# Kernel tuning notes

Hardware: AMD Instinct MI355X
Metric: run time of the kernel (lower is better)

Reference implementation:

```python
import jax, jax.numpy as jnp
import numpy as np

U = 356  # LSTM units

def _lstm(x, W, Wr, b, h0, c0):
    """Keras-style LSTM. x: [B,T,F]. Returns (hs [B,T,U], h [B,U], c [B,U])."""
    def step(carry, xt):
        h, c = carry
        z = xt @ W + h @ Wr + b            # [B, 4U], gate order i,f,g,o
        i, f, g, o = jnp.split(z, 4, axis=-1)
        c = jax.nn.sigmoid(f) * c + jax.nn.sigmoid(i) * jnp.tanh(g)
        h = jax.nn.sigmoid(o) * jnp.tanh(c)
        return (h, c), h
    (h, c), hs = jax.lax.scan(step, (h0, c0), jnp.swapaxes(x, 0, 1))
    return jnp.swapaxes(hs, 0, 1), h, c


def setup_inputs() -> dict:
    key = jax.random.key(0)
    ks = jax.random.split(key, 12)
    s = 0.05
    return {
        "x": jax.random.normal(ks[0], (8192, 7, 69), jnp.float32),
        "m": jax.random.normal(ks[1], (8192, 7, 45), jnp.float32),
        "enc_W": jax.random.normal(ks[2], (69, 4 * U), jnp.float32) * s,
        "enc_U": jax.random.normal(ks[3], (U, 4 * U), jnp.float32) * s,
        "enc_b": jnp.zeros((4 * U,), jnp.float32),
        "dec_W": jax.random.normal(ks[4], (45, 4 * U), jnp.float32) * s,
        "dec_U": jax.random.normal(ks[5], (U, 4 * U), jnp.float32) * s,
        "dec_b": jnp.zeros((4 * U,), jnp.float32),
        "W_map": jax.random.normal(ks[6], (7 * U, 1024), jnp.float32) * s,
        "b_map": jnp.zeros((1024,), jnp.float32),
        "W1": jax.random.normal(ks[7], (1024, 1024), jnp.float32) * s,
        "b1": jnp.zeros((1024,), jnp.float32),
        "W2": jax.random.normal(ks[8], (1024, 1024), jnp.float32) * s,
        "b2": jnp.zeros((1024,), jnp.float32),
        "W3": jax.random.normal(ks[9], (1024, 1024), jnp.float32) * s,
        "b3": jnp.zeros((1024,), jnp.float32),
        "W_out": jax.random.normal(ks[10], (1024, 168), jnp.float32) * s,
        "b_out": jnp.zeros((168,), jnp.float32),
    }


def reference(x, m, enc_W, enc_U, enc_b, dec_W, dec_U, dec_b,
              W_map, b_map, W1, b1, W2, b2, W3, b3, W_out, b_out):
    B = x.shape[0]
    h0 = jnp.zeros((B, U), x.dtype)
    c0 = jnp.zeros((B, U), x.dtype)
    # Encoder: only final states are used (dropout layers are identity at inference).
    _, s_h, s_c = _lstm(x, enc_W, enc_U, enc_b, h0, c0)
    # Decoder seeded with encoder states, returns full sequence [B,7,U].
    decoded, _, _ = _lstm(m, dec_W, dec_U, dec_b, s_h, s_c)
    f = decoded.reshape(B, -1)                     # [B, 7*356]
    h = jax.nn.relu(f @ W_map + b_map)
    h = jnp.tanh(h @ W1 + b1)
    h = jnp.tanh(h @ W2 + b2)
    h = jnp.tanh(h @ W3 + b3)
    return h @ W_out + b_out                        # [B, 168]
```

## Files before the change

### kernel.cpp

```cpp
#include <hip/hip_runtime.h>
#include <math.h>


using bf16x8 = __attribute__((ext_vector_type(8))) short;
using f32x4  = __attribute__((ext_vector_type(4))) float;

enum { EPI_NONE = 0, EPI_RELU = 1, EPI_TANH = 2 };

__device__ inline unsigned short f2bf(float f) {
    union { float f; unsigned u; } v; v.f = f;
    unsigned r = v.u + 0x7FFFu + ((v.u >> 16) & 1u);
    return (unsigned short)(r >> 16);
}
__device__ inline float sigf(float x) {
    return __fdividef(1.f, 1.f + __expf(-x));
}
__device__ inline float tanhfast(float x) {
    return 1.f - __fdividef(2.f, 1.f + __expf(2.f * x));
}

__device__ inline void gll16(const void* g, void* l) {
    __builtin_amdgcn_global_load_lds(
        (const __attribute__((address_space(1))) unsigned int*)(uintptr_t)g,
        (__attribute__((address_space(3))) unsigned int*)(unsigned int)(uintptr_t)l,
        16, 0, 0);
}

#define PROWS 32
#define PLDA  456

#define STAGEW(kkv)                                                            \
    _Pragma("unroll")                                                          \
    for (int r = 0; r < 12; ++r)                                               \
        gll16(Wt + (size_t)(kkv) * 49152 + (tid + r * 512) * 8,                \
              (void*)&Bs[(tid + r * 512) * 8]);

#define LOADB_LDS(dst)                                                         \
    _Pragma("unroll")                                                          \
    for (int ni = 0; ni < 12; ++ni)                                            \
        dst[ni] = *(const bf16x8*)&Bs[(w * 12 + ni) * 512 + lane * 8];

#define LOADA(dst, kkv)                                                        \
    _Pragma("unroll")                                                          \
    for (int mi = 0; mi < 2; ++mi)                                             \
        dst[mi] = *(const bf16x8*)&Ab[(mi * 16 + lm) * PLDA + (kkv) * 32       \
                                      + quad * 8];

#define MFMA12(aF, bW)                                                         \
    _Pragma("unroll")                                                          \
    for (int ni = 0; ni < 12; ++ni) {                                          \
        acc[0][ni] = __builtin_amdgcn_mfma_f32_16x16x32_bf16(                  \
            aF[0], bW[ni], acc[0][ni], 0, 0, 0);                               \
        acc[1][ni] = __builtin_amdgcn_mfma_f32_16x16x32_bf16(                  \
            aF[1], bW[ni], acc[1][ni], 0, 0, 0);                               \
    }

__global__ __attribute__((amdgpu_flat_work_group_size(512, 512),
                          amdgpu_waves_per_eu(2, 2)))
void lstm_persist(const float* __restrict__ x,
                  const float* __restrict__ m,
                  const unsigned short* __restrict__ WtE,
                  const unsigned short* __restrict__ WtD,
                  const float* __restrict__ bIE,
                  const float* __restrict__ bID,
                  unsigned short* __restrict__ dcd)
{
    __shared__ __attribute__((aligned(16))) unsigned short Ab[PROWS * PLDA];
    __shared__ __attribute__((aligned(16))) unsigned short Bs[49152];
    const int tid  = threadIdx.x;
    const int lane = tid & 63;
    const int w    = tid >> 6;
    const int lm   = lane & 15, quad = lane >> 4;
    const int brow = blockIdx.x * PROWS;
    const int kk0  = blockIdx.x % 14;

    for (int i = tid; i < PROWS * PLDA; i += 512) Ab[i] = 0;
    __syncthreads();
    for (int i = tid; i < PROWS * 69; i += 512) {
        const int r = i / 69, f = i - r * 69;
        Ab[r * PLDA + f] = f2bf(x[((size_t)(brow + r) * 7 + 0) * 69 + f]);
    }

    float creg[2][3][4] = {};
    float bI[3][4];

    for (int s = 0; s < 14; ++s) {
        const bool enc = (s < 7);
        const int t = enc ? s : s - 7;
        const unsigned short* Wt = enc ? WtE : WtD;

        if (s == 0 || s == 7) {
            const float* bsrc = enc ? bIE : bID;
            #pragma unroll
            for (int a = 0; a < 3; ++a)
                #pragma unroll
                for (int g = 0; g < 4; ++g)
                    bI[a][g] = bsrc[(3 * w + a) * 64 + g * 16 + lm];
        }

        STAGEW(kk0)
        __syncthreads();

        f32x4 acc[2][12] = {};
        #pragma unroll 1
        for (int kk = 0; kk < 14; ++kk) {
            const int kks = kk + kk0 - ((kk + kk0 >= 14) ? 14 : 0);
            bf16x8 bR[12], aF[2];
            LOADB_LDS(bR)
            LOADA(aF, kks)
            __syncthreads();
            if (kk < 13) {
                const int kkn = (kks == 13) ? 0 : kks + 1;
                STAGEW(kkn)
            }
            MFMA12(aF, bR)
            if (kk < 13) __syncthreads();
        }

        const int hoff = (s < 6) ? 69 : 45;
        #pragma unroll
        for (int mi = 0; mi < 2; ++mi)
            #pragma unroll
            for (int a = 0; a < 3; ++a) {
                const int u = (3 * w + a) * 16 + lm;
                const bool uok = (u < 356);
                #pragma unroll
                for (int r = 0; r < 4; ++r) {
                    const float zi = acc[mi][a * 4 + 0][r] + bI[a][0];
                    const float zf = acc[mi][a * 4 + 1][r] + bI[a][1];
                    const float zg = acc[mi][a * 4 + 2][r] + bI[a][2];
                    const float zo = acc[mi][a * 4 + 3][r] + bI[a][3];
                    const float cn = sigf(zf) * creg[mi][a][r]
                                   + sigf(zi) * tanhfast(zg);
                    creg[mi][a][r] = cn;
                    const unsigned short hb = f2bf(sigf(zo) * tanhfast(cn));
                    const int rl = mi * 16 + quad * 4 + r;
                    if (uok) {
                        if (s < 13) Ab[rl * PLDA + hoff + u] = hb;
                        if (!enc)
                            dcd[(size_t)(brow + rl) * 2496 + t * 356 + u] = hb;
                    }
                }
            }

        const int sn = s + 1;
        if (sn < 7) {
            for (int i = tid; i < PROWS * 69; i += 512) {
                const int r = i / 69, f = i - r * 69;
                Ab[r * PLDA + f] =
                    f2bf(x[((size_t)(brow + r) * 7 + sn) * 69 + f]);
            }
        } else if (sn < 14) {
            for (int i = tid; i < PROWS * 45; i += 512) {
                const int r = i / 45, f = i - r * 45;
                Ab[r * PLDA + f] =
                    f2bf(m[((size_t)(brow + r) * 7 + (sn - 7)) * 45 + f]);
            }
        }
    }
}


#define STAGE(A_, Bt_, K_, k0_, b_)                                            \
    {                                                                          \
        const int row = tid >> 2, kc = tid & 3;                                \
        gll16((A_)  + (size_t)(m0 + row) * (K_) + (k0_) + kc * 8,              \
              (void*)&As[b_][tid * 8]);                                        \
        gll16((Bt_) + (size_t)(n0 + row) * (K_) + (k0_) + kc * 8,              \
              (void*)&Bs[b_][tid * 8]);                                        \
    }

#define GEMM_CORE(A_, Bt_, K_)                                                 \
    STAGE(A_, Bt_, K_, 0, 0)                                                   \
    {                                                                          \
        const int niter = (K_) / 32;                                           \
        for (int it = 0; it < niter; ++it) {                                   \
            __syncthreads();                                                   \
            if (it + 1 < niter) {                                              \
                const int kn = (it + 1) * 32, bn = (it + 1) & 1;               \
                STAGE(A_, Bt_, K_, kn, bn)                                     \
            }                                                                  \
            const unsigned short* Asb = As[it & 1];                            \
            const unsigned short* Bsb = Bs[it & 1];                            \
            bf16x8 aF[2], bF[4];                                               \
            _Pragma("unroll")                                                  \
            for (int mi = 0; mi < 2; ++mi)                                     \
                aF[mi] = *(const bf16x8*)(Asb + (wr*32 + mi*16 + lm)*32 + quad*8);\
            _Pragma("unroll")                                                  \
            for (int ni = 0; ni < 4; ++ni)                                     \
                bF[ni] = *(const bf16x8*)(Bsb + (wc*64 + ni*16 + lm)*32 + quad*8);\
            _Pragma("unroll")                                                  \
            for (int mi = 0; mi < 2; ++mi)                                     \
                _Pragma("unroll")                                              \
                for (int ni = 0; ni < 4; ++ni)                                 \
                    acc[mi][ni] = __builtin_amdgcn_mfma_f32_16x16x32_bf16(     \
                        aF[mi], bF[ni], acc[mi][ni], 0, 0, 0);                 \
        }                                                                      \
    }

#define GEMM_PREAMBLE                                                          \
    __shared__ __attribute__((aligned(16))) unsigned short As[2][128 * 32];    \
    __shared__ __attribute__((aligned(16))) unsigned short Bs[2][128 * 32];    \
    const int tid  = threadIdx.x;                                              \
    const int lane = tid & 63;                                                 \
    const int w    = tid >> 6;                                       \
    const int wr   = w >> 1, wc = w & 1;                    \
    const int lm   = lane & 15, quad = lane >> 4;                              \
    const int m0   = blockIdx.x * 128, n0 = blockIdx.y * 128;                  \
    f32x4 acc[2][4] = {};

template <int EPI, int OUT_BF16, int NGUARD>
__global__ __launch_bounds__(512, 6)
void gemm_mfma(const unsigned short* __restrict__ A,
               const unsigned short* __restrict__ Bt,
               const float* __restrict__ bias,
               void* __restrict__ Cv, int ldc, int Nreal, int K)
{
    GEMM_PREAMBLE
    GEMM_CORE(A, Bt, K)
    #pragma unroll
    for (int mi = 0; mi < 2; ++mi)
        #pragma unroll
        for (int r = 0; r < 4; ++r) {
            const size_t row = m0 + wr * 32 + mi * 16 + quad * 4 + r;
            #pragma unroll
            for (int ni = 0; ni < 4; ++ni) {
                const int col = n0 + wc * 64 + ni * 16 + lm;
                if (!NGUARD || col < Nreal) {
                    float v = acc[mi][ni][r] + bias[col];
                    if (EPI == EPI_RELU) v = fmaxf(v, 0.f);
                    if (EPI == EPI_TANH) v = tanhfast(v);
                    if (OUT_BF16) ((unsigned short*)Cv)[row * ldc + col] = f2bf(v);
                    else          ((float*)Cv)[row * ldc + col] = v;
                }
            }
        }
}

struct PackArgs {
    const float *Wa0, *Wb0, *bias0; unsigned short* Wt0; float* bI0; int K10, K0, Kp0;
    const float *Wa1, *Wb1, *bias1; unsigned short* Wt1; float* bI1; int K11, K1, Kp1;
};
__global__ void pack_lstm2(PackArgs p)
{
    const float* Wa  = blockIdx.y ? p.Wa1  : p.Wa0;
    const float* Wb  = blockIdx.y ? p.Wb1  : p.Wb0;
    const float* bias= blockIdx.y ? p.bias1: p.bias0;
    unsigned short* Wt = blockIdx.y ? p.Wt1 : p.Wt0;
    float* biasI = blockIdx.y ? p.bI1 : p.bI0;
    const int K1 = blockIdx.y ? p.K11 : p.K10;
    const int K  = blockIdx.y ? p.K1  : p.K0;
    const int Kp = blockIdx.y ? p.Kp1 : p.Kp0;
    const int idx = blockIdx.x * 256 + threadIdx.x;
    if (idx >= 1536 * Kp) return;
    const int np = idx / Kp, k = idx - np * Kp;
    const int ub = np >> 6, g = (np >> 4) & 3, ul = np & 15;
    const int u = ub * 16 + ul;
    const bool valid = (u < 356);
    const int norig = g * 356 + u;
    float v = 0.f;
    if (valid && k < K)
        v = (k < K1) ? Wa[(size_t)k * 1424 + norig]
                     : Wb[(size_t)(k - K1) * 1424 + norig];
    const int wv = np / 192, rem = np - wv * 192;
    const int ni = rem >> 4, lmv = rem & 15;
    const int kkv = k >> 5, kq = k & 31;
    const int qd = kq >> 3, j = kq & 7;
    Wt[(size_t)kkv * 49152 + (size_t)(wv * 12 + ni) * 512 + (qd * 16 + lmv) * 8 + j]
        = f2bf(v);
    if (k == 0) biasI[np] = valid ? bias[norig] : 0.f;
}

__global__ void transpose_pack(const float* __restrict__ W, int K, int N,
                               unsigned short* __restrict__ Wt, int Kp, int Np)
{
    __shared__ float t[32][33];
    const int n0 = blockIdx.x * 32, k0 = blockIdx.y * 32;
    const int tx = threadIdx.x, ty = threadIdx.y;
    #pragma unroll
    for (int r = 0; r < 4; ++r) {
        const int k = k0 + ty + 8 * r, n = n0 + tx;
        t[ty + 8 * r][tx] = (k < K && n < N) ? W[(size_t)k * N + n] : 0.f;
    }
    __syncthreads();
    #pragma unroll
    for (int r = 0; r < 4; ++r) {
        const int k = k0 + tx, n = n0 + ty + 8 * r;
        if (k < Kp && n < Np) Wt[(size_t)n * Kp + k] = f2bf(t[tx][ty + 8 * r]);
    }
}

struct WP3 { const float *s0, *s1, *s2; unsigned short *d0, *d1, *d2; };
__global__ void transpose_pack3(WP3 p)
{
    __shared__ float t[32][33];
    const float* W = (blockIdx.z == 0) ? p.s0 : (blockIdx.z == 1) ? p.s1 : p.s2;
    unsigned short* Wt = (blockIdx.z == 0) ? p.d0 : (blockIdx.z == 1) ? p.d1 : p.d2;
    const int n0 = blockIdx.x * 32, k0 = blockIdx.y * 32;
    const int tx = threadIdx.x, ty = threadIdx.y;
    #pragma unroll
    for (int r = 0; r < 4; ++r)
        t[ty + 8 * r][tx] = W[(size_t)(k0 + ty + 8 * r) * 1024 + n0 + tx];
    __syncthreads();
    #pragma unroll
    for (int r = 0; r < 4; ++r)
        Wt[(size_t)(n0 + ty + 8 * r) * 1024 + k0 + tx] = f2bf(t[tx][ty + 8 * r]);
}

__global__ void zero_dcd_pad(unsigned short* __restrict__ dcd)
{
    const int i = blockIdx.x * 256 + threadIdx.x;
    if (i < 8192 * 4) dcd[(size_t)(i >> 2) * 2496 + 2492 + (i & 3)] = 0;
}

extern "C" void kernel_launch(void* const* d_in, const int* in_sizes, int n_in,
                              void* d_out, int out_size, void* d_ws, size_t ws_size,
                              hipStream_t stream)
{
    const float* x     = (const float*)d_in[0];
    const float* m     = (const float*)d_in[1];
    const float* enc_W = (const float*)d_in[2];
    const float* enc_U = (const float*)d_in[3];
    const float* enc_b = (const float*)d_in[4];
    const float* dec_W = (const float*)d_in[5];
    const float* dec_Um= (const float*)d_in[6];
    const float* dec_b = (const float*)d_in[7];
    const float* W_map = (const float*)d_in[8];
    const float* b_map = (const float*)d_in[9];
    const float* W1    = (const float*)d_in[10];
    const float* b1    = (const float*)d_in[11];
    const float* W2    = (const float*)d_in[12];
    const float* b2    = (const float*)d_in[13];
    const float* W3    = (const float*)d_in[14];
    const float* b3    = (const float*)d_in[15];
    const float* W_out = (const float*)d_in[16];
    const float* b_out = (const float*)d_in[17];
    float* out = (float*)d_out;

    const int B = 8192, FE = 69, FD = 45;
    const int KMP = 2496;

    char* ws = (char*)d_ws;
    size_t off = 0;
    auto alloc = [&](size_t bytes) -> void* {
        void* p = ws + off; off = (off + bytes + 255) & ~(size_t)255; return p;
    };
    unsigned short* WtE = (unsigned short*)alloc((size_t)1536 * 448 * 2);
    unsigned short* WtD = (unsigned short*)alloc((size_t)1536 * 448 * 2);
    unsigned short* WtM = (unsigned short*)alloc((size_t)1024 * KMP * 2);
    unsigned short* Wt1 = (unsigned short*)alloc((size_t)1024 * 1024 * 2);
    unsigned short* Wt2 = (unsigned short*)alloc((size_t)1024 * 1024 * 2);
    unsigned short* Wt3 = (unsigned short*)alloc((size_t)1024 * 1024 * 2);
    unsigned short* WtO = (unsigned short*)alloc((size_t)256 * 1024 * 2);
    float* bIE = (float*)alloc(1536 * 4);
    float* bID = (float*)alloc(1536 * 4);
    unsigned short* dcd = (unsigned short*)alloc((size_t)B * KMP * 2);
    unsigned short* a1  = (unsigned short*)alloc((size_t)B * 1024 * 2);
    unsigned short* a2  = (unsigned short*)alloc((size_t)B * 1024 * 2);

    PackArgs pa{enc_W, enc_U, enc_b, WtE, bIE, FE, FE + 356, 448,
                dec_W, dec_Um, dec_b, WtD, bID, FD, FD + 356, 448};
    pack_lstm2<<<dim3((1536 * 448 + 255) / 256, 2), 256, 0, stream>>>(pa);
    const dim3 tb(32, 8);
    transpose_pack<<<dim3(1024 / 32, KMP / 32), tb, 0, stream>>>(
        W_map, 2492, 1024, WtM, KMP, 1024);
    WP3 p3{W1, W2, W3, Wt1, Wt2, Wt3};
    transpose_pack3<<<dim3(32, 32, 3), tb, 0, stream>>>(p3);
    transpose_pack<<<dim3(256 / 32, 1024 / 32), tb, 0, stream>>>(
        W_out, 1024, 168, WtO, 1024, 256);
    zero_dcd_pad<<<(8192 * 4 + 255) / 256, 256, 0, stream>>>(dcd);

    lstm_persist<<<256, 512, 0, stream>>>(x, m, WtE, WtD, bIE, bID, dcd);

    gemm_mfma<EPI_RELU, 1, 0><<<dim3(64, 8), 512, 0, stream>>>(
        dcd, WtM, b_map, a1, 1024, 1024, KMP);
    gemm_mfma<EPI_TANH, 1, 0><<<dim3(64, 8), 512, 0, stream>>>(
        a1, Wt1, b1, a2, 1024, 1024, 1024);
    gemm_mfma<EPI_TANH, 1, 0><<<dim3(64, 8), 512, 0, stream>>>(
        a2, Wt2, b2, a1, 1024, 1024, 1024);
    gemm_mfma<EPI_TANH, 1, 0><<<dim3(64, 8), 512, 0, stream>>>(
        a1, Wt3, b3, a2, 1024, 1024, 1024);
    gemm_mfma<EPI_NONE, 0, 1><<<dim3(64, 2), 512, 0, stream>>>(
        a2, WtO, b_out, out, 168, 168, 1024);
}
```

Baseline: 621.8 us.

## Pipeline per-wave weight staging in three LDS chunks with vmcnt waits instead of barriers

Each wave now stages only its own slice of recurrent weights into LDS, split into three 4-tile chunks, and waits with s_waitcnt vmcnt rather than block-wide __syncthreads inside the K loop. Loads of the next k-slice chunks are issued while MFMAs on the current chunks run, which is meant to overlap global-to-LDS transfer with compute and drop per-iteration block barriers. This relies on the assumption that each wave reads only the LDS it wrote itself, and the hand-placed waitcnt counts must match the number of outstanding loads exactly.

```diff
diff --git a/kernel.cpp b/kernel.cpp
--- a/kernel.cpp
+++ b/kernel.cpp
@@ -29,16 +29,18 @@
 #define PROWS 32
 #define PLDA  456
 
-#define STAGEW(kkv)                                                            \
+#define STAGE_CHUNK(bufv, kkv, partv)                                          \
     _Pragma("unroll")                                                          \
-    for (int r = 0; r < 12; ++r)                                               \
-        gll16(Wt + (size_t)(kkv) * 49152 + (tid + r * 512) * 8,                \
-              (void*)&Bs[(tid + r * 512) * 8]);
-
-#define LOADB_LDS(dst)                                                         \
+    for (int q = 0; q < 4; ++q)                                                \
+        gll16(Wt + (size_t)(kkv) * 49152 + (w * 12 + (partv) * 4 + q) * 512    \
+                  + lane * 8,                                                  \
+              (void*)&Bs[((w * 3 + (bufv)) * 4 + q) * 512 + lane * 8]);
+
+#define LOADB4(dst, bufv)                                                      \
     _Pragma("unroll")                                                          \
-    for (int ni = 0; ni < 12; ++ni)                                            \
-        dst[ni] = *(const bf16x8*)&Bs[(w * 12 + ni) * 512 + lane * 8];
+    for (int q = 0; q < 4; ++q)                                                \
+        dst[q] = *(const bf16x8*)&Bs[((w * 3 + (bufv)) * 4 + q) * 512          \
+                                     + lane * 8];
 
 #define LOADA(dst, kkv)                                                        \
     _Pragma("unroll")                                                          \
@@ -46,14 +48,18 @@
         dst[mi] = *(const bf16x8*)&Ab[(mi * 16 + lm) * PLDA + (kkv) * 32       \
                                       + quad * 8];
 
-#define MFMA12(aF, bW)                                                         \
+#define MFMA8(partv, bRv)                                                      \
     _Pragma("unroll")                                                          \
-    for (int ni = 0; ni < 12; ++ni) {                                          \
-        acc[0][ni] = __builtin_amdgcn_mfma_f32_16x16x32_bf16(                  \
-            aF[0], bW[ni], acc[0][ni], 0, 0, 0);                               \
-        acc[1][ni] = __builtin_amdgcn_mfma_f32_16x16x32_bf16(                  \
-            aF[1], bW[ni], acc[1][ni], 0, 0, 0);                               \
-    }
+    for (int q = 0; q < 4; ++q) {                                              \
+        acc[0][(partv) * 4 + q] = __builtin_amdgcn_mfma_f32_16x16x32_bf16(     \
+            aF[0], bRv[q], acc[0][(partv) * 4 + q], 0, 0, 0);                  \
+        acc[1][(partv) * 4 + q] = __builtin_amdgcn_mfma_f32_16x16x32_bf16(     \
+            aF[1], bRv[q], acc[1][(partv) * 4 + q], 0, 0, 0);                  \
+    }
+
+#define VMWAIT(n)                                                              \
+    asm volatile("s_waitcnt vmcnt(" #n ")" ::: "memory");                      \
+    __builtin_amdgcn_sched_barrier(0);
 
 __global__ __attribute__((amdgpu_flat_work_group_size(512, 512),
                           amdgpu_waves_per_eu(2, 2)))
@@ -98,24 +104,43 @@
                     bI[a][g] = bsrc[(3 * w + a) * 64 + g * 16 + lm];
         }
 
-        STAGEW(kk0)
         __syncthreads();
 
         f32x4 acc[2][12] = {};
-        #pragma unroll 1
-        for (int kk = 0; kk < 14; ++kk) {
-            const int kks = kk + kk0 - ((kk + kk0 >= 14) ? 14 : 0);
-            bf16x8 bR[12], aF[2];
-            LOADB_LDS(bR)
-            LOADA(aF, kks)
-            __syncthreads();
-            if (kk < 13) {
-                const int kkn = (kks == 13) ? 0 : kks + 1;
-                STAGEW(kkn)
+        {
+            STAGE_CHUNK(0, kk0, 0)
+            STAGE_CHUNK(1, kk0, 1)
+            int kkc = kk0;
+            #pragma unroll 1
+            for (int i = 0; i < 14; ++i) {
+                const int kkn = (kkc == 13) ? 0 : kkc + 1;
+                bf16x8 aF[2], bR[4];
+                STAGE_CHUNK(2, kkc, 2)
+                VMWAIT(8)
+                LOADA(aF, kkc)
+                LOADB4(bR, 0)
+                MFMA8(0, bR)
+                if (i < 13) {
+                    STAGE_CHUNK(0, kkn, 0)
+                    VMWAIT(8)
+                } else {
+                    VMWAIT(4)
+                }
+                LOADB4(bR, 1)
+                MFMA8(1, bR)
+                if (i < 13) {
+                    STAGE_CHUNK(1, kkn, 1)
+                    VMWAIT(8)
+                } else {
+                    VMWAIT(0)
+                }
+                LOADB4(bR, 2)
+                MFMA8(2, bR)
+                kkc = kkn;
             }
-            MFMA12(aF, bR)
-            if (kk < 13) __syncthreads();
         }
+
+        __syncthreads();
 
         const int hoff = (s < 6) ? 69 : 45;
         #pragma unroll
```

New measurement: 570.2 us. 1.09x faster.
